# Kernel optimization log

Hardware: AMD Instinct MI355X
Metric: run time of the kernel (lower is better)

Reference implementation:

```python
import jax, jax.numpy as jnp
import numpy as np

EPS = 1e-12  # torch F.normalize default eps


def setup_inputs() -> dict:
    key = jax.random.key(0)
    k1, k2, k3 = jax.random.split(key, 3)
    b, c, H, W = 16, 384, 48, 48
    heads = 8
    x = jax.random.normal(k1, (b, c, H, W), dtype=jnp.float32)
    # torch Linear weight init scale ~ 1/sqrt(fan_in); use scaled normals
    w_qkv = jax.random.normal(k2, (c, 3 * c), dtype=jnp.float32) / np.sqrt(c)
    temperature = jnp.ones((1, heads, 1, 1), dtype=jnp.float32)
    w_out = jax.random.normal(k3, (c, c), dtype=jnp.float32) / np.sqrt(c)
    b_out = jnp.zeros((c,), dtype=jnp.float32)
    return {"x": x, "w_qkv": w_qkv, "temperature": temperature,
            "w_out": w_out, "b_out": b_out}


def reference(x, w_qkv, temperature, w_out, b_out):
    b, c, H, W = x.shape
    h = temperature.shape[1]
    d = c // h
    n = H * W
    # b c h w -> b n c
    xt = x.reshape(b, c, n).transpose(0, 2, 1)
    qkv = xt @ w_qkv  # [b, n, 3c]
    q, k, v = jnp.split(qkv, 3, axis=-1)
    q = q.reshape(b, n, h, d).transpose(0, 2, 1, 3)  # b h n d
    k = k.reshape(b, n, h, d).transpose(0, 2, 3, 1)  # b h d n
    v = v.reshape(b, n, h, d).transpose(0, 2, 1, 3)  # b h n d
    # L2 normalize over the token axis (n): q over dim=-2, k over dim=-1
    q = q / jnp.maximum(jnp.sqrt(jnp.sum(q * q, axis=-2, keepdims=True)), EPS)
    k = k / jnp.maximum(jnp.sqrt(jnp.sum(k * k, axis=-1, keepdims=True)), EPS)
    k = k * temperature
    # cross-covariance attention over channels: [b, h, d, d]
    attn = jnp.einsum('bhpn,bhnq->bhpq', k, q)
    attn = jax.nn.softmax(attn, axis=-1)
    out = jnp.einsum('bhnp,bhpq->bhnq', v, attn)  # [b, h, n, d]
    out = out.transpose(0, 2, 1, 3).reshape(b, n, c)  # b n (h d)
    out = out @ w_out + b_out
    # b n c -> b c h w
    out = out.transpose(0, 2, 1).reshape(b, c, H, W)
    return out
```

## Files before the change

kernel.cpp:

```cpp
#include <hip/hip_runtime.h>
#include <cstdint>

typedef __attribute__((ext_vector_type(8))) short short8;
typedef __attribute__((ext_vector_type(4))) float f32x4;
typedef unsigned int u32;
typedef unsigned short u16;

#define NTOK 2304
#define CDIM 384

__device__ __forceinline__ u16 f2bf(float f) {
    u32 u = __builtin_bit_cast(u32, f);
    u32 r = (u + 0x7FFFu + ((u >> 16) & 1u)) >> 16;
    return (u16)r;
}
__device__ __forceinline__ float bf2f(u32 h) {
    u32 u = h << 16;
    return __builtin_bit_cast(float, u);
}

__global__ __launch_bounds__(256) void transpose_all(
    const float* __restrict__ x, const float* __restrict__ w_qkv,
    const float* __restrict__ w_out,
    u16* __restrict__ xT, u16* __restrict__ xbf,
    u16* __restrict__ wqkvT, u16* __restrict__ wv, u16* __restrict__ woutT)
{
    __shared__ float tile[64][65];
    const int bz = blockIdx.z;
    const float* src; int Csz; char* dT; char* dC = nullptr;
    int dcCol0 = 0; long dcRowB = 0;
    if (bz < 16) {
        src = x + (long)bz * 384 * 2304; Csz = 2304;
        dT = (char*)(xT + (long)bz * 2304 * 384);
        dC = (char*)(xbf + (long)bz * 384 * 2304);
        dcCol0 = 0; dcRowB = 2304 * 2;
    } else if (bz == 16) {
        if (blockIdx.x >= 18) return;
        src = w_qkv; Csz = 1152;
        dT = (char*)wqkvT; dC = (char*)wv; dcCol0 = 768; dcRowB = 768;
    } else {
        if (blockIdx.x >= 6) return;
        src = w_out; Csz = 384;
        dT = (char*)woutT;
    }
    const int c0 = blockIdx.x * 64;
    const int k0 = blockIdx.y * 64;
    const int t = threadIdx.x;
    const int rr = t >> 2, cc4 = (t & 3) * 16;

    const float* srow = src + (long)(k0 + rr) * Csz + c0 + cc4;
#pragma unroll
    for (int i = 0; i < 4; ++i) {
        float4 v = *(const float4*)(srow + i * 4);
        tile[rr][cc4 + i*4 + 0] = v.x;
        tile[rr][cc4 + i*4 + 1] = v.y;
        tile[rr][cc4 + i*4 + 2] = v.z;
        tile[rr][cc4 + i*4 + 3] = v.w;
    }
    __syncthreads();

    {
        char* drow = dT + (long)(c0 + rr) * (CDIM * 2);
        const int sw = (rr & 7) << 4;
#pragma unroll
        for (int half = 0; half < 2; ++half) {
            u32 pk[4];
#pragma unroll
            for (int i = 0; i < 4; ++i) {
                float v0 = tile[cc4 + half*8 + 2*i][rr];
                float v1 = tile[cc4 + half*8 + 2*i + 1][rr];
                pk[i] = (u32)f2bf(v0) | ((u32)f2bf(v1) << 16);
            }
            uint4 q; q.x = pk[0]; q.y = pk[1]; q.z = pk[2]; q.w = pk[3];
            const int inrow = (k0 + cc4 + half*8) * 2;
            *(uint4*)(drow + (inrow ^ sw)) = q;
        }
    }
    if (dC && c0 >= dcCol0) {
        char* drow = dC + (long)(k0 + rr) * dcRowB;
        const int sw = (rr & 7) << 4;
#pragma unroll
        for (int half = 0; half < 2; ++half) {
            u32 pk[4];
#pragma unroll
            for (int i = 0; i < 4; ++i) {
                float v0 = tile[rr][cc4 + half*8 + 2*i];
                float v1 = tile[rr][cc4 + half*8 + 2*i + 1];
                pk[i] = (u32)f2bf(v0) | ((u32)f2bf(v1) << 16);
            }
            uint4 q; q.x = pk[0]; q.y = pk[1]; q.z = pk[2]; q.w = pk[3];
            const int inrow = (c0 - dcCol0 + cc4 + half*8) * 2;
            *(uint4*)(drow + (inrow ^ sw)) = q;
        }
    }
}

template<int MODE, int KT, int KROW>
__device__ __forceinline__ void gemm_core(
    const u16* __restrict__ Ab, const u16* __restrict__ Bb,
    char* __restrict__ Obase, int m0, int n0, int ostride,
    const float* __restrict__ bias, u16* As, u16* Bs)
{
    constexpr int KB = KROW * 128;
    const int t = threadIdx.x;
    const int w = t >> 6, l = t & 63;
    const int wm = (w >> 1) * 64, wn = (w & 1) * 64;
    const int srow = t >> 3;
    const int scol = (t & 7) * 16;
    f32x4 acc[4][4] = {};

    auto stage = [&](int buf, int kt) {
        const int kbyte = kt * 128;
#pragma unroll
        for (int i = 0; i < 4; ++i) {
            const int row = srow + i * 32;
            const long so = (long)row * KB + kbyte + scol;
            const int d = buf * 16384 + (i * 256 + t) * 16;
            __builtin_amdgcn_global_load_lds(
                (const __attribute__((address_space(1))) u32*)((const char*)Ab + so),
                (__attribute__((address_space(3))) u32*)((char*)As + d), 16, 0, 0);
            __builtin_amdgcn_global_load_lds(
                (const __attribute__((address_space(1))) u32*)((const char*)Bb + so),
                (__attribute__((address_space(3))) u32*)((char*)Bs + d), 16, 0, 0);
        }
    };

    stage(0, 0);
    __syncthreads();
    int cur = 0;
#pragma unroll 1
    for (int kt = 0; kt < KT; ++kt) {
        if (kt < KT - 1) stage(cur ^ 1, kt + 1);
        const char* Ac = (const char*)As + cur * 16384;
        const char* Bc = (const char*)Bs + cur * 16384;
#pragma unroll
        for (int kk = 0; kk < 2; ++kk) {
            short8 af[4], bfr[4];
#pragma unroll
            for (int mi = 0; mi < 4; ++mi) {
                const int m = wm + mi * 16 + (l & 15);
                const int off = m * 128 + ((kk * 64 + (l >> 4) * 16) ^ ((m & 7) << 4));
                af[mi] = *(const short8*)(Ac + off);
            }
#pragma unroll
            for (int ni = 0; ni < 4; ++ni) {
                const int n = wn + ni * 16 + (l & 15);
                const int off = n * 128 + ((kk * 64 + (l >> 4) * 16) ^ ((n & 7) << 4));
                bfr[ni] = *(const short8*)(Bc + off);
            }
#pragma unroll
            for (int mi = 0; mi < 4; ++mi)
#pragma unroll
                for (int ni = 0; ni < 4; ++ni)
                    acc[mi][ni] = __builtin_amdgcn_mfma_f32_16x16x32_bf16(
                        af[mi], bfr[ni], acc[mi][ni], 0, 0, 0);
        }
        __syncthreads();
        cur ^= 1;
    }

    if (MODE == 0) {
        u16* O = (u16*)Obase;
#pragma unroll
        for (int mi = 0; mi < 4; ++mi) {
            const int mb = m0 + wm + mi * 16 + (l >> 4) * 4;
#pragma unroll
            for (int ni = 0; ni < 4; ++ni) {
                const int n = n0 + wn + ni * 16 + (l & 15);
#pragma unroll
                for (int r = 0; r < 4; ++r)
                    O[(long)(mb + r) * ostride + n] = f2bf(acc[mi][ni][r]);
            }
        }
    } else if (MODE == 1) {
        float* O = (float*)Obase;
#pragma unroll
        for (int mi = 0; mi < 4; ++mi) {
            const int mb = m0 + wm + mi * 16 + (l >> 4) * 4;
#pragma unroll
            for (int r = 0; r < 4; ++r) {
                const float bb = bias[mb + r];
#pragma unroll
                for (int ni = 0; ni < 4; ++ni) {
                    const int n = n0 + wn + ni * 16 + (l & 15);
                    O[(long)(mb + r) * ostride + n] = acc[mi][ni][r] + bb;
                }
            }
        }
    } else if (MODE == 3) {
        float* O = (float*)Obase;
#pragma unroll
        for (int mi = 0; mi < 4; ++mi) {
            const int mb = m0 + wm + mi * 16 + (l >> 4) * 4;
#pragma unroll
            for (int r = 0; r < 4; ++r)
#pragma unroll
                for (int ni = 0; ni < 4; ++ni) {
                    const int n = n0 + wn + ni * 16 + (l & 15);
                    O[(long)(mb + r) * ostride + n] = acc[mi][ni][r];
                }
        }
    } else {
#pragma unroll
        for (int mi = 0; mi < 4; ++mi) {
            const int mb = m0 + wm + mi * 16 + (l >> 4) * 4;
#pragma unroll
            for (int ni = 0; ni < 4; ++ni) {
                const int n = n0 + wn + ni * 16 + (l & 15);
#pragma unroll
                for (int r = 0; r < 4; ++r) {
                    const int m = mb + r;
                    const long byteoff = (long)m * (ostride * 2) +
                        (((long)n * 2) ^ ((m & 7) << 4));
                    *(u16*)(Obase + byteoff) = f2bf(acc[mi][ni][r]);
                }
            }
        }
    }
}

__global__ __launch_bounds__(256) void g_partial(
    const u16* __restrict__ xbf, float* __restrict__ Gp)
{
    __shared__ __attribute__((aligned(16))) u16 As[2][128 * 64];
    __shared__ __attribute__((aligned(16))) u16 Bs[2][128 * 64];
    const int lid = blockIdx.x;
    const int swzid = (lid & 7) * 54 + (lid >> 3);
    const int chunk = swzid / 144;
    const int rem2 = swzid % 144;
    const int b = rem2 / 9, rem = rem2 % 9;
    const int m0 = (rem % 3) * 128, n0 = (rem / 3) * 128;
    const u16* xb = xbf + (long)b * 384 * NTOK + chunk * 768;
    gemm_core<3, 12, 36>(xb + (long)m0 * NTOK, xb + (long)n0 * NTOK,
                         (char*)(Gp + ((long)chunk * 16 + b) * 147456),
                         m0, n0, 384, nullptr, &As[0][0], &Bs[0][0]);
}

__global__ __launch_bounds__(256) void g_reduce(
    const float* __restrict__ Gp, u16* __restrict__ Gs)
{
    const int idx = blockIdx.x * 256 + threadIdx.x;
    const long e8 = (long)idx * 8;
    const int b = (int)(e8 / 147456);
    const int rmn = (int)(e8 % 147456);
    const int r = rmn / 384, n = rmn % 384;
    const float* p0 = Gp + (long)b * 147456 + rmn;
    const float* p1 = p0 + 16L * 147456;
    const float* p2 = p1 + 16L * 147456;
    float4 a0 = *(const float4*)p0, a1 = *(const float4*)(p0 + 4);
    float4 b0 = *(const float4*)p1, b1 = *(const float4*)(p1 + 4);
    float4 c0 = *(const float4*)p2, c1 = *(const float4*)(p2 + 4);
    float s[8];
    s[0] = a0.x + b0.x + c0.x; s[1] = a0.y + b0.y + c0.y;
    s[2] = a0.z + b0.z + c0.z; s[3] = a0.w + b0.w + c0.w;
    s[4] = a1.x + b1.x + c1.x; s[5] = a1.y + b1.y + c1.y;
    s[6] = a1.z + b1.z + c1.z; s[7] = a1.w + b1.w + c1.w;
    uint4 q;
    q.x = (u32)f2bf(s[0]) | ((u32)f2bf(s[1]) << 16);
    q.y = (u32)f2bf(s[2]) | ((u32)f2bf(s[3]) << 16);
    q.z = (u32)f2bf(s[4]) | ((u32)f2bf(s[5]) << 16);
    q.w = (u32)f2bf(s[6]) | ((u32)f2bf(s[7]) << 16);
    *(uint4*)((char*)Gs + (long)b * 294912 + r * 768 +
              ((n * 2) ^ ((r & 7) << 4))) = q;
}

__device__ __forceinline__ void sm_fold_core(
    const u16* __restrict__ Tp, const u16* __restrict__ wT,
    const float* __restrict__ temp, const u16* __restrict__ woutT,
    u16* __restrict__ W2T, int h, int b, char* shb)
{
    float* Sp  = (float*)shb;
    float* S   = (float*)(shb + 36864);
    float* invk = (float*)(shb + 46272);
    float* invq = (float*)(shb + 46464);
    u16* Sbf = (u16*)(shb + 46656);

    const int t = threadIdx.x;
    const int w = t >> 6, l = t & 63, lr = l & 15, lk = (l >> 4) * 8;
    const int h48 = h * 48;

    const u16* Tk = Tp + ((long)b * 768 + 384 + h48) * CDIM;
    {
        f32x4 acc[3][3] = {};
#pragma unroll
        for (int ks = 0; ks < 3; ++ks) {
            const int k0 = w * 96 + ks * 32 + lk;
            short8 af[3], bfr[3];
#pragma unroll
            for (int mi = 0; mi < 3; ++mi)
                af[mi] = *(const short8*)(Tk + (long)(mi * 16 + lr) * CDIM + k0);
#pragma unroll
            for (int ni = 0; ni < 3; ++ni) {
                const int row = h48 + ni * 16 + lr;
                const char* base = (const char*)wT + (long)row * 768;
                bfr[ni] = *(const short8*)(base + ((k0 * 2) ^ ((row & 7) << 4)));
            }
#pragma unroll
            for (int mi = 0; mi < 3; ++mi)
#pragma unroll
                for (int ni = 0; ni < 3; ++ni)
                    acc[mi][ni] = __builtin_amdgcn_mfma_f32_16x16x32_bf16(
                        af[mi], bfr[ni], acc[mi][ni], 0, 0, 0);
        }
#pragma unroll
        for (int mi = 0; mi < 3; ++mi)
#pragma unroll
            for (int ni = 0; ni < 3; ++ni)
#pragma unroll
                for (int r = 0; r < 4; ++r)
                    Sp[w * 2304 + (mi * 16 + (l >> 4) * 4 + r) * 48 + ni * 16 + lr]
                        = acc[mi][ni][r];
    }
    if (t < 96) {
        const int ch = (t < 48) ? (h48 + t) : (384 + h48 + (t - 48));
        const u16* trow = Tp + ((long)b * 768 + ch) * CDIM;
        const char* wrow = (const char*)wT + (long)ch * 768;
        const int sw = (ch & 7) << 4;
        float s = 0.f;
#pragma unroll 4
        for (int i = 0; i < 48; ++i) {
            short8 tv = *(const short8*)(trow + i * 8);
            short8 wv = *(const short8*)(wrow + ((i * 16) ^ sw));
#pragma unroll
            for (int e = 0; e < 8; ++e)
                s += bf2f((u16)tv[e]) * bf2f((u16)wv[e]);
        }
        float inv = 1.0f / fmaxf(sqrtf(fmaxf(s, 0.f)), 1e-12f);
        if (t < 48) invq[t] = inv; else invk[t - 48] = inv;
    }
    __syncthreads();
    for (int idx = t; idx < 2304; idx += 256) {
        const int p = idx / 48, q = idx % 48;
        S[p * 49 + q] = Sp[idx] + Sp[2304 + idx] + Sp[4608 + idx] + Sp[6912 + idx];
    }
    __syncthreads();
    if (t < 48) {
        const float sc = temp[h] * invk[t];
        float row[48];
        float mx = -1e30f;
#pragma unroll 8
        for (int q = 0; q < 48; ++q) {
            row[q] = S[t * 49 + q] * sc * invq[q];
            mx = fmaxf(mx, row[q]);
        }
        float ssum = 0.f;
#pragma unroll 8
        for (int q = 0; q < 48; ++q) {
            row[q] = __expf(row[q] - mx);
            ssum += row[q];
        }
        float inv = 1.0f / ssum;
        const int sw = (t & 7) << 4;
#pragma unroll
        for (int g = 0; g < 8; ++g) {
            u32 pk[4];
#pragma unroll
            for (int e = 0; e < 4; ++e) {
                const int q0 = g * 8 + 2 * e;
                float v0 = (q0 < 48) ? row[q0] * inv : 0.f;
                float v1 = (q0 + 1 < 48) ? row[q0 + 1] * inv : 0.f;
                pk[e] = (u32)f2bf(v0) | ((u32)f2bf(v1) << 16);
            }
            uint4 qv; qv.x = pk[0]; qv.y = pk[1]; qv.z = pk[2]; qv.w = pk[3];
            *(uint4*)((char*)Sbf + t * 128 + ((g * 16) ^ sw)) = qv;
        }
    }
    __syncthreads();
    {
        const char* SbfB = (const char*)Sbf;
        const int jw = w * 96;
        f32x4 fac[3][6] = {};
#pragma unroll
        for (int ks = 0; ks < 2; ++ks) {
            const int ka = ks * 64 + (l >> 4) * 16;
            const int kb = h * 96 + ka;
            short8 af[3], bfr[6];
#pragma unroll
            for (int mi = 0; mi < 3; ++mi) {
                const int p = mi * 16 + lr;
                af[mi] = *(const short8*)(SbfB + p * 128 + (ka ^ ((p & 7) << 4)));
            }
#pragma unroll
            for (int ni = 0; ni < 6; ++ni) {
                const int j = jw + ni * 16 + lr;
                bfr[ni] = *(const short8*)((const char*)woutT + (long)j * 768 +
                                           (kb ^ ((j & 7) << 4)));
            }
#pragma unroll
            for (int mi = 0; mi < 3; ++mi)
#pragma unroll
                for (int ni = 0; ni < 6; ++ni)
                    fac[mi][ni] = __builtin_amdgcn_mfma_f32_16x16x32_bf16(
                        af[mi], bfr[ni], fac[mi][ni], 0, 0, 0);
        }
        char* Wb = (char*)W2T + (long)b * 294912;
#pragma unroll
        for (int mi = 0; mi < 3; ++mi)
#pragma unroll
            for (int ni = 0; ni < 6; ++ni)
#pragma unroll
                for (int r = 0; r < 4; ++r) {
                    const int p = mi * 16 + (l >> 4) * 4 + r;
                    const int j = jw + ni * 16 + lr;
                    const long byteoff = (long)j * 768 +
                        (((h48 + p) * 2) ^ ((j & 7) << 4));
                    *(u16*)(Wb + byteoff) = f2bf(fac[mi][ni][r]);
                }
    }
}

__global__ __launch_bounds__(256) void sm_fold_kernel(
    const u16* __restrict__ Tp, const u16* __restrict__ wT,
    const float* __restrict__ temp, const u16* __restrict__ woutT,
    u16* __restrict__ W2T)
{
    __shared__ __attribute__((aligned(16))) char shb[52800];
    sm_fold_core(Tp, wT, temp, woutT, W2T, blockIdx.x, blockIdx.y, shb);
}

template<int MODE, int KT, int GX, int GY>
__global__ __launch_bounds__(256) void mfma_gemm(
    const u16* __restrict__ A, long aBatch,
    const u16* __restrict__ Bm, long bBatch,
    void* __restrict__ Ovoid, long oBatch, int ostride,
    const float* __restrict__ bias)
{
    constexpr int KE  = KT * 64;
    constexpr int NWG = GX * GY * 16;
    __shared__ __attribute__((aligned(16))) u16 As[2][128 * 64];
    __shared__ __attribute__((aligned(16))) u16 Bs[2][128 * 64];

    const int lid = blockIdx.x + GX * (blockIdx.y + GY * blockIdx.z);
    const int swzid = (lid & 7) * (NWG / 8) + (lid >> 3);
    const int b   = swzid / (GX * GY);
    const int rem = swzid % (GX * GY);
    const int m0 = (rem % GX) * 128, n0 = (rem / GX) * 128;

    char* Obase = (char*)Ovoid + (long)b * oBatch * (MODE == 1 ? 4 : 2);
    gemm_core<MODE, KT, KT>(A + (long)b * aBatch + (long)m0 * KE,
                            Bm + (long)b * bBatch + (long)n0 * KE,
                            Obase, m0, n0, ostride, bias,
                            &As[0][0], &Bs[0][0]);
}

extern "C" void kernel_launch(void* const* d_in, const int* in_sizes, int n_in,
                              void* d_out, int out_size, void* d_ws, size_t ws_size,
                              hipStream_t stream) {
    const float* x     = (const float*)d_in[0];
    const float* w_qkv = (const float*)d_in[1];
    const float* temp  = (const float*)d_in[2];
    const float* w_out = (const float*)d_in[3];
    const float* b_out = (const float*)d_in[4];
    float* out = (float*)d_out;

    char* ws = (char*)d_ws;
    const size_t SZ_XBF = 16UL * 384 * 2304 * 2;
    const size_t SZ_XT  = 16UL * 2304 * 384 * 2;
    const size_t SZ_WQT = 1152UL * 384 * 2;
    const size_t SZ_WV  = 384UL * 384 * 2;
    const size_t SZ_WOT = 384UL * 384 * 2 + 256;
    const size_t SZ_GP  = 3UL * 16 * 384 * 384 * 4;
    const size_t SZ_G   = 16UL * 384 * 384 * 2;
    const size_t SZ_TP  = 16UL * 768 * 384 * 2;
    const size_t SZ_W2  = 16UL * 384 * 384 * 2;

    size_t off = 0;
    u16*   xbf   = (u16*)(ws + off); off += SZ_XBF;
    u16*   xT    = (u16*)(ws + off); off += SZ_XT;
    u16*   wqkvT = (u16*)(ws + off); off += SZ_WQT;
    u16*   wv    = (u16*)(ws + off); off += SZ_WV;
    u16*   woutT = (u16*)(ws + off); off += SZ_WOT;
    float* Gp    = (float*)(ws + off); off += SZ_GP;
    u16*   Gs    = (u16*)(ws + off); off += SZ_G;
    u16*   Tp    = (u16*)(ws + off); off += SZ_TP;
    u16*   W2T   = (u16*)(ws + off); off += SZ_W2;
    u16*   W3    = (u16*)(ws + off);

    transpose_all<<<dim3(36, 6, 18), 256, 0, stream>>>(
        x, w_qkv, w_out, xT, xbf, wqkvT, wv, woutT);
    g_partial<<<432, 256, 0, stream>>>(xbf, Gp);
    g_reduce<<<1152, 256, 0, stream>>>(Gp, Gs);
    mfma_gemm<0, 6, 6, 3><<<dim3(6, 3, 16), 256, 0, stream>>>(
        wqkvT, 0L, Gs, 384L * 384, Tp, 768L * 384, 384, nullptr);
    sm_fold_kernel<<<dim3(8, 16), 256, 0, stream>>>(
        Tp, wqkvT, temp, woutT, W2T);
    mfma_gemm<2, 6, 3, 3><<<dim3(3, 3, 16), 256, 0, stream>>>(
        W2T, 384L * 384, wv, 0L, W3, 384L * 384, 384, nullptr);
    mfma_gemm<1, 6, 3, 18><<<dim3(3, 18, 16), 256, 0, stream>>>(
        W3, 384L * 384, xT, 384L * 2304, out, 384L * 2304, 2304, b_out);
}
```

Baseline: 111.5 us.

## Exploit Gram matrix symmetry: compute upper-triangle tiles, mirror in reduce

The Gram matrix x·xᵀ is symmetric, so the partial-GEMM now computes only the 6 upper-triangular 128x128 tiles per batch instead of all 9, splitting the token axis into 4 chunks instead of 3 to keep the block count high. The reduce kernel sums the 4 partials per 64x64 upper-triangle tile, stages the tile in shared memory, and writes both it and its transpose to the swizzled bf16 output. This cuts MFMA work and partial-buffer traffic by about a third, at the cost of one extra partial to reduce and a larger workspace.

Result: no change. 110.2 us (-1.1%).

```diff
diff --git a/kernel.cpp b/kernel.cpp
--- a/kernel.cpp
+++ b/kernel.cpp
@@ -225,43 +225,88 @@
     __shared__ __attribute__((aligned(16))) u16 As[2][128 * 64];
     __shared__ __attribute__((aligned(16))) u16 Bs[2][128 * 64];
     const int lid = blockIdx.x;
-    const int swzid = (lid & 7) * 54 + (lid >> 3);
-    const int chunk = swzid / 144;
-    const int rem2 = swzid % 144;
-    const int b = rem2 / 9, rem = rem2 % 9;
-    const int m0 = (rem % 3) * 128, n0 = (rem / 3) * 128;
-    const u16* xb = xbf + (long)b * 384 * NTOK + chunk * 768;
-    gemm_core<3, 12, 36>(xb + (long)m0 * NTOK, xb + (long)n0 * NTOK,
-                         (char*)(Gp + ((long)chunk * 16 + b) * 147456),
-                         m0, n0, 384, nullptr, &As[0][0], &Bs[0][0]);
+    const int swzid = (lid & 7) * 48 + (lid >> 3);
+    const int chunk = swzid / 96;
+    const int rem2 = swzid % 96;
+    const int b = rem2 / 6;
+    const int tile = rem2 % 6;
+    const int ti = (tile < 3) ? 0 : ((tile < 5) ? 1 : 2);
+    const int tj = (tile < 3) ? tile : ((tile < 5) ? tile - 2 : 2);
+    const int m0 = ti * 128, n0 = tj * 128;
+    const u16* xb = xbf + (long)b * 384 * NTOK + chunk * 576;
+    gemm_core<3, 9, 36>(xb + (long)m0 * NTOK, xb + (long)n0 * NTOK,
+                        (char*)(Gp + ((long)chunk * 16 + b) * 147456),
+                        m0, n0, 384, nullptr, &As[0][0], &Bs[0][0]);
 }
 
 __global__ __launch_bounds__(256) void g_reduce(
     const float* __restrict__ Gp, u16* __restrict__ Gs)
 {
-    const int idx = blockIdx.x * 256 + threadIdx.x;
-    const long e8 = (long)idx * 8;
-    const int b = (int)(e8 / 147456);
-    const int rmn = (int)(e8 % 147456);
-    const int r = rmn / 384, n = rmn % 384;
-    const float* p0 = Gp + (long)b * 147456 + rmn;
-    const float* p1 = p0 + 16L * 147456;
-    const float* p2 = p1 + 16L * 147456;
-    float4 a0 = *(const float4*)p0, a1 = *(const float4*)(p0 + 4);
-    float4 b0 = *(const float4*)p1, b1 = *(const float4*)(p1 + 4);
-    float4 c0 = *(const float4*)p2, c1 = *(const float4*)(p2 + 4);
-    float s[8];
-    s[0] = a0.x + b0.x + c0.x; s[1] = a0.y + b0.y + c0.y;
-    s[2] = a0.z + b0.z + c0.z; s[3] = a0.w + b0.w + c0.w;
-    s[4] = a1.x + b1.x + c1.x; s[5] = a1.y + b1.y + c1.y;
-    s[6] = a1.z + b1.z + c1.z; s[7] = a1.w + b1.w + c1.w;
-    uint4 q;
-    q.x = (u32)f2bf(s[0]) | ((u32)f2bf(s[1]) << 16);
-    q.y = (u32)f2bf(s[2]) | ((u32)f2bf(s[3]) << 16);
-    q.z = (u32)f2bf(s[4]) | ((u32)f2bf(s[5]) << 16);
-    q.w = (u32)f2bf(s[6]) | ((u32)f2bf(s[7]) << 16);
-    *(uint4*)((char*)Gs + (long)b * 294912 + r * 768 +
-              ((n * 2) ^ ((r & 7) << 4))) = q;
+    __shared__ float tile[64][65];
+    const int b = blockIdx.y;
+    int u = blockIdx.x, i64 = 0;
+    while (u >= 6 - i64) { u -= 6 - i64; ++i64; }
+    const int j64 = i64 + u;
+
+    const int t = threadIdx.x;
+    const int rr = t >> 2, cc4 = (t & 3) * 16;
+
+    const float* base = Gp + (long)b * 147456 +
+                        (long)(i64 * 64 + rr) * 384 + j64 * 64 + cc4;
+    float acc[16];
+#pragma unroll
+    for (int i = 0; i < 4; ++i) {
+        float4 v = *(const float4*)(base + i * 4);
+        acc[i*4+0] = v.x; acc[i*4+1] = v.y; acc[i*4+2] = v.z; acc[i*4+3] = v.w;
+    }
+#pragma unroll
+    for (int c = 1; c < 4; ++c) {
+        const float* p = base + (long)c * 16 * 147456;
+#pragma unroll
+        for (int i = 0; i < 4; ++i) {
+            float4 v = *(const float4*)(p + i * 4);
+            acc[i*4+0] += v.x; acc[i*4+1] += v.y;
+            acc[i*4+2] += v.z; acc[i*4+3] += v.w;
+        }
+    }
+#pragma unroll
+    for (int i = 0; i < 16; ++i) tile[rr][cc4 + i] = acc[i];
+    __syncthreads();
+
+    char* Gb = (char*)Gs + (long)b * 294912;
+    const int sw = (rr & 7) << 4;
+    {
+        char* drow = Gb + (long)(i64 * 64 + rr) * 768;
+#pragma unroll
+        for (int half = 0; half < 2; ++half) {
+            u32 pk[4];
+#pragma unroll
+            for (int i = 0; i < 4; ++i) {
+                float v0 = tile[rr][cc4 + half*8 + 2*i];
+                float v1 = tile[rr][cc4 + half*8 + 2*i + 1];
+                pk[i] = (u32)f2bf(v0) | ((u32)f2bf(v1) << 16);
+            }
+            uint4 q; q.x = pk[0]; q.y = pk[1]; q.z = pk[2]; q.w = pk[3];
+            const int inrow = (j64 * 64 + cc4 + half*8) * 2;
+            *(uint4*)(drow + (inrow ^ sw)) = q;
+        }
+    }
+    {
+        char* drow = Gb + (long)(j64 * 64 + rr) * 768;
+#pragma unroll
+        for (int half = 0; half < 2; ++half) {
+            u32 pk[4];
+#pragma unroll
+            for (int i = 0; i < 4; ++i) {
+                float v0 = tile[cc4 + half*8 + 2*i][rr];
+                float v1 = tile[cc4 + half*8 + 2*i + 1][rr];
+                pk[i] = (u32)f2bf(v0) | ((u32)f2bf(v1) << 16);
+            }
+            uint4 q; q.x = pk[0]; q.y = pk[1]; q.z = pk[2]; q.w = pk[3];
+            const int inrow = (i64 * 64 + cc4 + half*8) * 2;
+            *(uint4*)(drow + (inrow ^ sw)) = q;
+        }
+    }
 }
 
 __device__ __forceinline__ void sm_fold_core(
@@ -459,7 +504,7 @@
     const size_t SZ_WQT = 1152UL * 384 * 2;
     const size_t SZ_WV  = 384UL * 384 * 2;
     const size_t SZ_WOT = 384UL * 384 * 2 + 256;
-    const size_t SZ_GP  = 3UL * 16 * 384 * 384 * 4;
+    const size_t SZ_GP  = 4UL * 16 * 384 * 384 * 4;
     const size_t SZ_G   = 16UL * 384 * 384 * 2;
     const size_t SZ_TP  = 16UL * 768 * 384 * 2;
     const size_t SZ_W2  = 16UL * 384 * 384 * 2;
@@ -478,8 +523,8 @@
 
     transpose_all<<<dim3(36, 6, 18), 256, 0, stream>>>(
         x, w_qkv, w_out, xT, xbf, wqkvT, wv, woutT);
-    g_partial<<<432, 256, 0, stream>>>(xbf, Gp);
-    g_reduce<<<1152, 256, 0, stream>>>(Gp, Gs);
+    g_partial<<<384, 256, 0, stream>>>(xbf, Gp);
+    g_reduce<<<dim3(21, 16), 256, 0, stream>>>(Gp, Gs);
     mfma_gemm<0, 6, 6, 3><<<dim3(6, 3, 16), 256, 0, stream>>>(
         wqkvT, 0L, Gs, 384L * 384, Tp, 768L * 384, 384, nullptr);
     sm_fold_kernel<<<dim3(8, 16), 256, 0, stream>>>(
```
